# Optimization experiments

Hardware: AMD Instinct MI355X
Metric: run time of the kernel (lower is better)

Reference implementation:

```python
import jax, jax.numpy as jnp
import numpy as np

B, N, C = 4, 8192, 512
H, D = 8, 64          # heads, dim_head; inner_dim = H*D = 512
EPS = 1e-6


def setup_inputs() -> dict:
    key = jax.random.key(0)
    k1, k2, k3 = jax.random.split(key, 3)
    x = jax.random.normal(k1, (B, N, C), dtype=jnp.float32)
    # fan-in scaled init so sigmoid features are not saturated
    W_qkv = jax.random.normal(k2, (3 * H * D, C), dtype=jnp.float32) * (C ** -0.5)
    W_proj = jax.random.normal(k3, (C, H * D), dtype=jnp.float32) * ((H * D) ** -0.5)
    b_proj = jnp.zeros((C,), dtype=jnp.float32)
    return {"x": x, "W_qkv": W_qkv, "W_proj": W_proj, "b_proj": b_proj}


def reference(x, W_qkv, W_proj, b_proj):
    b, n, c = x.shape
    qkv = x @ W_qkv.T                                   # [B,N,3HD]
    q, k, v = jnp.split(qkv, 3, axis=-1)
    to_heads = lambda t: t.reshape(b, n, H, D).transpose(0, 2, 1, 3)  # [B,H,N,D]
    q, k, v = to_heads(q), to_heads(k), to_heads(v)
    q = jax.nn.sigmoid(q)
    k = jax.nn.sigmoid(k)
    scale = D ** -0.5
    v = v / ((scale * c) // H)                           # torch: v / (scale*C // heads) == v / 8.0

    k_sum = k.sum(axis=2)                                # [B,H,D]
    q_sum = q.sum(axis=2)                                # [B,H,D]
    # sink/source incoming-outgoing flow (per token): [B,H,N]
    sink_incoming = 1.0 / (((q + EPS) * (k_sum + EPS)[:, :, None, :]).sum(-1) + EPS)
    source_outgoing = 1.0 / (((k + EPS) * (q_sum + EPS)[:, :, None, :]).sum(-1) + EPS)
    conserved_sink = ((q + EPS) * ((k * source_outgoing[..., None]).sum(2) + EPS)[:, :, None, :]).sum(-1) + EPS
    conserved_source = ((k + EPS) * ((q * sink_incoming[..., None]).sum(2) + EPS)[:, :, None, :]).sum(-1) + EPS
    conserved_source = jnp.clip(conserved_source, -1.0, 1.0)

    sink_allocation = jax.nn.sigmoid(conserved_sink * (float(q.shape[2]) / float(k.shape[2])))
    source_competition = jax.nn.softmax(conserved_source, axis=-1) * float(k.shape[2])

    # linear attention: k^T @ v then q @ (kv); kv is tiny [B,H,D,D]
    kv = jnp.einsum('bhnd,bhne->bhde', k, v * source_competition[..., None])
    x_update = jnp.einsum('bhnd,bhde->bhne', q, kv) * sink_incoming[..., None] * sink_allocation[..., None]

    out = x_update.transpose(0, 2, 1, 3).reshape(b, n, H * D)
    return out @ W_proj.T + b_proj
```

## Files before the change

### kernel.cpp

```cpp
#include <hip/hip_runtime.h>
#include <hip/hip_bf16.h>

typedef __attribute__((ext_vector_type(8))) short short8;
typedef __attribute__((ext_vector_type(4))) float f32x4;

constexpr int cB = 4, cN = 8192, cC = 512, cH = 8, cD = 64;
constexpr int cM = cB * cN;
constexpr int cHD = cH * cD;
constexpr int cBH = cB * cH;
constexpr float kEPS = 1e-6f;
constexpr int KV_SPLIT = 32;

__device__ __forceinline__ ushort rne_bf16(float f) {
  unsigned u = __float_as_uint(f);
  u += 0x7fffu + ((u >> 16) & 1u);
  return (ushort)(u >> 16);
}
__device__ __forceinline__ float b2f(ushort u) {
  return __uint_as_float((unsigned)u << 16);
}

__global__ __launch_bounds__(256) void round_w(const float* __restrict__ src,
    ushort* __restrict__ w, int n4) {
  int i = blockIdx.x * 256 + threadIdx.x;
  if (i >= n4) return;
  float4 v = reinterpret_cast<const float4*>(src)[i];
  ushort4 h;
  h.x = rne_bf16(v.x); h.y = rne_bf16(v.y);
  h.z = rne_bf16(v.z); h.w = rne_bf16(v.w);
  reinterpret_cast<ushort4*>(w)[i] = h;
}

template<int EPI, int NY>
__global__ __launch_bounds__(256) void gemm_mfma(
    const ushort* __restrict__ Ab, const ushort* __restrict__ Wb, int bstride,
    const float* __restrict__ bias,
    void* __restrict__ o0v, void* __restrict__ o1v, void* __restrict__ o2v,
    float* __restrict__ qsum, float* __restrict__ ksum) {
  constexpr int NT = cC / 32;
  __shared__ ushort AhS[2][128 * 32];
  __shared__ ushort BhS[2][128 * 32];
  float* colsum = (float*)AhS;
  const int t = threadIdx.x;
  const int wave = t >> 6, lane = t & 63;
  const int wm = wave >> 1, wn = wave & 1;
  const int l15 = lane & 15, lg = lane >> 4;

  const int raw = blockIdx.y * gridDim.x + blockIdx.x;
  const int q8 = (int)(gridDim.x * NY) >> 3;
  const int wg2 = (raw & 7) * q8 + (raw >> 3);
  const int rowchunk = wg2 / NY, ycol = wg2 - rowchunk * NY;
  const int row0 = rowchunk * 128, col0 = ycol * 128;
  const size_t wofs = (size_t)(row0 >> 13) * (size_t)bstride;

  f32x4 acc[4][4] = {};

  const int srow = lane >> 2, sunit = lane & 3;

#define STAGE_T(basep, base0, dstbuf, k0)                                       \
  _Pragma("unroll")                                                             \
  for (int hh = 0; hh < 2; ++hh) {                                              \
    const int rr_ = wave * 32 + hh * 16 + srow;                                 \
    const int sw = sunit ^ ((rr_ >> 1) & 3);                                    \
    const size_t goff = (size_t)(base0 + rr_) * cC + (k0) + sw * 8;             \
    __builtin_amdgcn_global_load_lds(                                           \
        (const __attribute__((address_space(1))) void*)(basep + goff),          \
        (__attribute__((address_space(3))) void*)(&dstbuf[(wave * 32 + hh * 16) * 32]), \
        16, 0, 0);                                                              \
  }

  STAGE_T(Ab, row0, AhS[0], 0);
  STAGE_T((Wb + wofs), col0, BhS[0], 0);
  STAGE_T(Ab, row0, AhS[1], 32);
  STAGE_T((Wb + wofs), col0, BhS[1], 32);

  int cur = 0;
  for (int kt = 0; kt < NT; ++kt) {
    if (kt < NT - 1) asm volatile("s_waitcnt vmcnt(4)" ::: "memory");
    else             asm volatile("s_waitcnt vmcnt(0)" ::: "memory");
    __builtin_amdgcn_s_barrier();
    short8 ah[4], bhf[4];
    #pragma unroll
    for (int mi = 0; mi < 4; ++mi) {
      const int r = wm * 64 + mi * 16 + l15;
      ah[mi] = *reinterpret_cast<const short8*>(
          &AhS[cur][r * 32 + (lg ^ ((r >> 1) & 3)) * 8]);
    }
    #pragma unroll
    for (int ni = 0; ni < 4; ++ni) {
      const int c = wn * 64 + ni * 16 + l15;
      bhf[ni] = *reinterpret_cast<const short8*>(
          &BhS[cur][c * 32 + (lg ^ ((c >> 1) & 3)) * 8]);
    }
    asm volatile("s_waitcnt lgkmcnt(0)" ::: "memory");
    __builtin_amdgcn_sched_barrier(0);
    __builtin_amdgcn_s_barrier();
    if (kt + 2 < NT) {
      STAGE_T(Ab, row0, AhS[cur], (kt + 2) * 32);
      STAGE_T((Wb + wofs), col0, BhS[cur], (kt + 2) * 32);
    }
    #pragma unroll
    for (int ni = 0; ni < 4; ++ni)
      #pragma unroll
      for (int mi = 0; mi < 4; ++mi)
        acc[mi][ni] = __builtin_amdgcn_mfma_f32_16x16x32_bf16(ah[mi], bhf[ni], acc[mi][ni], 0, 0, 0);
    cur ^= 1;
  }
#undef STAGE_T

  const bool qk_block = (EPI == 0) && (ycol < 8);
  if (qk_block) {
    if (t < 128) colsum[t] = 0.f;
    __syncthreads();
  }

  float csum[4] = {};
  #pragma unroll
  for (int mi = 0; mi < 4; ++mi) {
    #pragma unroll
    for (int r = 0; r < 4; ++r) {
      const int m = row0 + wm * 64 + mi * 16 + lg * 4 + r;
      #pragma unroll
      for (int ni = 0; ni < 4; ++ni) {
        const int col = col0 + wn * 64 + ni * 16 + l15;
        const float val = acc[mi][ni][r];
        if (EPI == 0) {
          const int which = col >> 9;
          const int c2 = col & 511;
          const int h = c2 >> 6, d = c2 & 63;
          const int bb = m >> 13, n = m & 8191;
          const size_t idx = (((size_t)(bb * cH + h)) * cN + n) * cD + d;
          if (which < 2) {
            const float sv = 1.f / (1.f + __expf(-val));
            if (which == 0) ((ushort*)o0v)[idx] = rne_bf16(sv);
            else            ((ushort*)o1v)[idx] = rne_bf16(sv);
            csum[ni] += sv;
          } else {
            ((ushort*)o2v)[idx] = rne_bf16(val * 0.125f);
          }
        } else {
          ((float*)o0v)[(size_t)m * cC + col] = val + bias[col];
        }
      }
    }
  }
  if (qk_block) {
    #pragma unroll
    for (int ni = 0; ni < 4; ++ni)
      atomicAdd(&colsum[wn * 64 + ni * 16 + l15], csum[ni]);
    __syncthreads();
    if (t < 128) {
      const int col = col0 + t;
      const int c2 = col & 511;
      const int h = c2 >> 6, d = c2 & 63;
      const int bb = row0 >> 13;
      float* tgt = (col < 512) ? qsum : ksum;
      atomicAdd(&tgt[(bb * cH + h) * cD + d], colsum[t]);
    }
  }
}

__global__ __launch_bounds__(256) void k34_flow(const ushort* __restrict__ q,
      const ushort* __restrict__ k, const float* __restrict__ qsum,
      const float* __restrict__ ksum, float* __restrict__ si,
      float* __restrict__ Sq, float* __restrict__ Sk) {
  const int bh = blockIdx.x;
  const int n0 = blockIdx.y * 256;
  const int t = threadIdx.x;
  const int wave = t >> 6, lane = t & 63;
  const int g = lane >> 4, j = lane & 15;
  const ushort* qb = q + (size_t)bh * cN * cD;
  const ushort* kb = k + (size_t)bh * cN * cD;
  const float4 ks4 = *(const float4*)&ksum[bh * 64 + j * 4];
  const float4 qs4 = *(const float4*)&qsum[bh * 64 + j * 4];
  const float ksd[4] = {ks4.x + kEPS, ks4.y + kEPS, ks4.z + kEPS, ks4.w + kEPS};
  const float qsd[4] = {qs4.x + kEPS, qs4.y + kEPS, qs4.z + kEPS, qs4.w + kEPS};
  float aSq[4] = {}, aSk[4] = {};
  for (int i = 0; i < 16; ++i) {
    const int n = n0 + wave * 64 + i * 4 + g;
    const ushort4 qu = *(const ushort4*)&qb[(size_t)n * cD + j * 4];
    const ushort4 ku = *(const ushort4*)&kb[(size_t)n * cD + j * 4];
    const float qa[4] = {b2f(qu.x), b2f(qu.y), b2f(qu.z), b2f(qu.w)};
    const float ka[4] = {b2f(ku.x), b2f(ku.y), b2f(ku.z), b2f(ku.w)};
    float t1 = 0.f, t2 = 0.f;
    #pragma unroll
    for (int c = 0; c < 4; ++c) {
      t1 = fmaf(qa[c] + kEPS, ksd[c], t1);
      t2 = fmaf(ka[c] + kEPS, qsd[c], t2);
    }
    #pragma unroll
    for (int off = 1; off < 16; off <<= 1) {
      t1 += __shfl_xor(t1, off);
      t2 += __shfl_xor(t2, off);
    }
    const float si_n = 1.f / (t1 + kEPS);
    const float so_n = 1.f / (t2 + kEPS);
    if (j == 0) si[(size_t)bh * cN + n] = si_n;
    #pragma unroll
    for (int c = 0; c < 4; ++c) {
      aSq[c] = fmaf(qa[c], si_n, aSq[c]);
      aSk[c] = fmaf(ka[c], so_n, aSk[c]);
    }
  }
  #pragma unroll
  for (int c = 0; c < 4; ++c) {
    aSq[c] += __shfl_xor(aSq[c], 16); aSq[c] += __shfl_xor(aSq[c], 32);
    aSk[c] += __shfl_xor(aSk[c], 16); aSk[c] += __shfl_xor(aSk[c], 32);
  }
  __shared__ float sAq[4][64], sAk[4][64];
  if (g == 0) {
    #pragma unroll
    for (int c = 0; c < 4; ++c) { sAq[wave][j * 4 + c] = aSq[c]; sAk[wave][j * 4 + c] = aSk[c]; }
  }
  __syncthreads();
  if (t < 64) {
    atomicAdd(&Sq[bh * 64 + t], sAq[0][t] + sAq[1][t] + sAq[2][t] + sAq[3][t]);
    atomicAdd(&Sk[bh * 64 + t], sAk[0][t] + sAk[1][t] + sAk[2][t] + sAk[3][t]);
  }
}

__global__ __launch_bounds__(256) void k45_kv(const ushort* __restrict__ kk_,
      const ushort* __restrict__ vv, const float* __restrict__ Sq,
      float* __restrict__ kvpart, float* __restrict__ zpart) {
  const int bh = blockIdx.x;
  const int y = blockIdx.y;
  constexpr int ROWS = cN / KV_SPLIT;
  const int n0 = y * ROWS;
  const int t = threadIdx.x;
  const int d = t & 63, eb = t >> 6;
  const int g = t >> 4, j = t & 15;
  const int sr = t >> 4, sc = (t & 15) * 4;
  const ushort* kb = kk_ + (size_t)bh * cN * cD;
  const ushort* vb = vv + (size_t)bh * cN * cD;
  const float4 sq4 = *(const float4*)&Sq[bh * 64 + j * 4];
  const float SqE[4] = {sq4.x + kEPS, sq4.y + kEPS, sq4.z + kEPS, sq4.w + kEPS};
  __shared__ float ks[32][64];
  __shared__ float vs[32][64];
  __shared__ float evs[32];
  __shared__ float zl[16];
  float acc[16] = {};
  float zacc = 0.f;
  ushort4 pk0 = *(const ushort4*)&kb[(size_t)(n0 + sr) * cD + sc];
  ushort4 pk1 = *(const ushort4*)&kb[(size_t)(n0 + 16 + sr) * cD + sc];
  ushort4 pv0 = *(const ushort4*)&vb[(size_t)(n0 + sr) * cD + sc];
  ushort4 pv1 = *(const ushort4*)&vb[(size_t)(n0 + 16 + sr) * cD + sc];
  for (int c0 = 0; c0 < ROWS; c0 += 32) {
    __syncthreads();
    *(float4*)&ks[sr][sc]      = make_float4(b2f(pk0.x), b2f(pk0.y), b2f(pk0.z), b2f(pk0.w));
    *(float4*)&ks[sr + 16][sc] = make_float4(b2f(pk1.x), b2f(pk1.y), b2f(pk1.z), b2f(pk1.w));
    *(float4*)&vs[sr][sc]      = make_float4(b2f(pv0.x), b2f(pv0.y), b2f(pv0.z), b2f(pv0.w));
    *(float4*)&vs[sr + 16][sc] = make_float4(b2f(pv1.x), b2f(pv1.y), b2f(pv1.z), b2f(pv1.w));
    __syncthreads();
    if (c0 + 32 < ROWS) {
      pk0 = *(const ushort4*)&kb[(size_t)(n0 + c0 + 32 + sr) * cD + sc];
      pk1 = *(const ushort4*)&kb[(size_t)(n0 + c0 + 48 + sr) * cD + sc];
      pv0 = *(const ushort4*)&vb[(size_t)(n0 + c0 + 32 + sr) * cD + sc];
      pv1 = *(const ushort4*)&vb[(size_t)(n0 + c0 + 48 + sr) * cD + sc];
    }
    #pragma unroll
    for (int rr = 0; rr < 2; ++rr) {
      const int r = g * 2 + rr;
      const float4 kk4 = *(const float4*)&ks[r][j * 4];
      float tt = 0.f;
      tt = fmaf(kk4.x + kEPS, SqE[0], tt);
      tt = fmaf(kk4.y + kEPS, SqE[1], tt);
      tt = fmaf(kk4.z + kEPS, SqE[2], tt);
      tt = fmaf(kk4.w + kEPS, SqE[3], tt);
      #pragma unroll
      for (int off = 1; off < 16; off <<= 1) tt += __shfl_xor(tt, off);
      if (j == 0) {
        const float cs = fminf(fmaxf(tt + kEPS, -1.f), 1.f);
        const float e = __expf(cs);
        evs[r] = e;
        zacc += e;
      }
    }
    __syncthreads();
    #pragma unroll
    for (int r = 0; r < 32; ++r) {
      const float kd = ks[r][d] * evs[r];
      #pragma unroll
      for (int j2 = 0; j2 < 16; ++j2)
        acc[j2] = fmaf(kd, vs[r][eb * 16 + j2], acc[j2]);
    }
  }
  if (j == 0) zl[g] = zacc;
  __syncthreads();
  if (t == 0) {
    float z = 0.f;
    #pragma unroll
    for (int i = 0; i < 16; ++i) z += zl[i];
    zpart[y * cBH + bh] = z;
  }
  float* kvb = kvpart + ((size_t)y * cBH + bh) * 4096 + d * 64 + eb * 16;
  #pragma unroll
  for (int j2 = 0; j2 < 16; ++j2) kvb[j2] = acc[j2];
}

__global__ __launch_bounds__(256) void k5r_reduce(const float* __restrict__ kvpart,
      const float* __restrict__ zpart, float* __restrict__ kvm, float* __restrict__ Zb) {
  const int bh = blockIdx.x;
  const int yq = blockIdx.y;
  const int t = threadIdx.x;
  for (int i = yq * 1024 + t; i < (yq + 1) * 1024; i += 256) {
    float s = 0.f;
    #pragma unroll
    for (int yy = 0; yy < KV_SPLIT; ++yy)
      s += kvpart[((size_t)yy * cBH + bh) * 4096 + i];
    kvm[(size_t)bh * 4096 + i] = s;
  }
  if (yq == 0 && t == 0) {
    float z = 0.f;
    #pragma unroll
    for (int yy = 0; yy < KV_SPLIT; ++yy) z += zpart[yy * cBH + bh];
    Zb[bh] = z;
  }
}

__global__ __launch_bounds__(256) void kvw_build(const float* __restrict__ kvm,
      const float* __restrict__ Wproj, const float* __restrict__ Zb,
      ushort* __restrict__ kvw) {
  const int bh = blockIdx.x;
  const int c0 = blockIdx.y * 128;
  const int b = bh >> 3, h = bh & 7;
  const int t = threadIdx.x;
  __shared__ float kvs[64][64];
  for (int i = t; i < 4096; i += 256)
    kvs[i >> 6][i & 63] = kvm[(size_t)bh * 4096 + i];
  __syncthreads();
  const float zs = (float)cN / Zb[bh];
  const int cl = t & 127, half = t >> 7;
  const int c = c0 + cl;
  float acc[32] = {};
  for (int ec = 0; ec < 64; ec += 8) {
    float w[8];
    #pragma unroll
    for (int e = 0; e < 8; ++e)
      w[e] = Wproj[(size_t)c * cHD + h * 64 + ec + e];
    #pragma unroll
    for (int d = 0; d < 32; ++d)
      #pragma unroll
      for (int e = 0; e < 8; ++e)
        acc[d] = fmaf(kvs[half * 32 + d][ec + e], w[e], acc[d]);
  }
  ushort* dst = kvw + (size_t)b * cC * cHD + (size_t)c * cC + h * 64 + half * 32;
  #pragma unroll
  for (int d = 0; d < 32; ++d) dst[d] = rne_bf16(acc[d] * zs);
}

__global__ __launch_bounds__(256) void k6c_scaleq(const ushort* __restrict__ q,
      const float* __restrict__ si, const float* __restrict__ Sk,
      ushort* __restrict__ xq) {
  const int bh = blockIdx.x;
  const int b = bh >> 3, head = bh & 7;
  const int n0 = blockIdx.y * 256;
  const int t = threadIdx.x;
  const int wave = t >> 6, lane = t & 63;
  const int g = lane >> 4, j = lane & 15;
  const ushort* qb = q + (size_t)bh * cN * cD;
  const float4 sk4 = *(const float4*)&Sk[bh * 64 + j * 4];
  const float SkE[4] = {sk4.x + kEPS, sk4.y + kEPS, sk4.z + kEPS, sk4.w + kEPS};
  for (int i = 0; i < 16; ++i) {
    const int n = n0 + wave * 64 + i * 4 + g;
    const ushort4 qu = *(const ushort4*)&qb[(size_t)n * cD + j * 4];
    const float q0 = b2f(qu.x), q1 = b2f(qu.y), q2 = b2f(qu.z), q3 = b2f(qu.w);
    float t2 = 0.f;
    t2 = fmaf(q0 + kEPS, SkE[0], t2);
    t2 = fmaf(q1 + kEPS, SkE[1], t2);
    t2 = fmaf(q2 + kEPS, SkE[2], t2);
    t2 = fmaf(q3 + kEPS, SkE[3], t2);
    #pragma unroll
    for (int off = 1; off < 16; off <<= 1) t2 += __shfl_xor(t2, off);
    const float sa_n = 1.f / (1.f + __expf(-(t2 + kEPS)));
    const float s = si[(size_t)bh * cN + n] * sa_n;
    ushort4 hh;
    hh.x = rne_bf16(q0 * s);
    hh.y = rne_bf16(q1 * s);
    hh.z = rne_bf16(q2 * s);
    hh.w = rne_bf16(q3 * s);
    const size_t m = (size_t)b * cN + n;
    *(ushort4*)&xq[m * cC + head * 64 + j * 4] = hh;
  }
}

extern "C" void kernel_launch(void* const* d_in, const int* in_sizes, int n_in,
                              void* d_out, int out_size, void* d_ws, size_t ws_size,
                              hipStream_t stream) {
  (void)in_sizes; (void)n_in; (void)out_size;
  const float* x     = (const float*)d_in[0];
  const float* Wqkv  = (const float*)d_in[1];
  const float* Wproj = (const float*)d_in[2];
  const float* bproj = (const float*)d_in[3];
  float* out = (float*)d_out;
  float* ws  = (float*)d_ws;

  const size_t SLAB = (size_t)cBH * cN * cD;
  const size_t OFF_Q   = 0;
  const size_t OFF_K   = SLAB;
  const size_t OFF_V   = 2 * SLAB;
  const size_t OFF_ACC = 3 * SLAB;
  const size_t ACC_FLOATS = 2048 * 4 + 32 + (size_t)cBH * cD * cD;
  const size_t OFF_R   = OFF_ACC + ACC_FLOATS;
  const size_t R_FLOATS = (size_t)3 * cHD * cC;
  const size_t TOTAL   = OFF_R + R_FLOATS;
  if (ws_size < TOTAL * sizeof(float)) return;

  ushort* q16 = (ushort*)(ws + OFF_Q);
  ushort* k16 = (ushort*)(ws + OFF_K);
  ushort* v16 = (ushort*)(ws + OFF_V);
  ushort* xq  = (ushort*)(ws + OFF_V + SLAB / 2);
  float* ksum = ws + OFF_ACC;
  float* qsum = ksum + 2048;
  float* Sk   = ksum + 4096;
  float* Sq   = ksum + 6144;
  float* Zb   = ksum + 8192;
  float* kvm  = ksum + 8224;

  ushort* wq  = (ushort*)(ws + OFF_R);
  float*  si  = ws + OFF_R;
  ushort* kvw = (ushort*)(ws + OFF_R + (size_t)cBH * cN);

  ushort* xs    = (ushort*)out;
  float* kvpart = out + (size_t)8 * 1024 * 1024;
  float* zpart  = kvpart + (size_t)KV_SPLIT * cBH * 4096;

  hipMemsetAsync(ksum, 0, ACC_FLOATS * sizeof(float), stream);

  round_w<<<(3 * cHD * cC / 4 + 255) / 256, 256, 0, stream>>>(Wqkv, wq, 3 * cHD * cC / 4);
  round_w<<<((size_t)cM * cC / 4 + 255) / 256, 256, 0, stream>>>(x, xs, cM * cC / 4);
  gemm_mfma<0, 12><<<dim3(cM / 128, (3 * cHD) / 128), 256, 0, stream>>>(
      xs, wq, 0, nullptr, q16, k16, v16, qsum, ksum);
  k34_flow<<<dim3(cBH, cN / 256), 256, 0, stream>>>(q16, k16, qsum, ksum, si, Sq, Sk);
  k45_kv<<<dim3(cBH, KV_SPLIT), 256, 0, stream>>>(k16, v16, Sq, kvpart, zpart);
  k5r_reduce<<<dim3(cBH, 4), 256, 0, stream>>>(kvpart, zpart, kvm, Zb);
  kvw_build<<<dim3(cBH, 4), 256, 0, stream>>>(kvm, Wproj, Zb, kvw);
  k6c_scaleq<<<dim3(cBH, cN / 256), 256, 0, stream>>>(q16, si, Sk, xq);
  gemm_mfma<1, 4><<<dim3(cM / 128, cHD / 128), 256, 0, stream>>>(
      xq, kvw, cC * cHD, bproj, out, nullptr, nullptr, nullptr, nullptr);
}
```

Before: 238.2 us.

## Give each wave private LDS tiles to remove block barriers in GEMM loop

Each wave now stages its own 64-row A slice and 64-column B slice into a private LDS region, replacing the shared double-buffered 128x32 tiles and the two block-wide barriers per K step. Because waves share no data, only a vmcnt wait is needed before reading, and the next tile is prefetched after the LDS reads finish. The cost is that A and B tiles are fetched twice each (paired waves duplicate loads), global traffic per block doubles, and only one stage of prefetch remains, so load latency is less hidden.

```diff
diff --git a/kernel.cpp b/kernel.cpp
--- a/kernel.cpp
+++ b/kernel.cpp
@@ -38,9 +38,8 @@
     void* __restrict__ o0v, void* __restrict__ o1v, void* __restrict__ o2v,
     float* __restrict__ qsum, float* __restrict__ ksum) {
   constexpr int NT = cC / 32;
-  __shared__ ushort AhS[2][128 * 32];
-  __shared__ ushort BhS[2][128 * 32];
-  float* colsum = (float*)AhS;
+  __shared__ ushort LDSu[4 * 4096];
+  float* colsum = (float*)LDSu;
   const int t = threadIdx.x;
   const int wave = t >> 6, lane = t & 63;
   const int wm = wave >> 1, wn = wave & 1;
@@ -56,60 +55,60 @@
   f32x4 acc[4][4] = {};
 
   const int srow = lane >> 2, sunit = lane & 3;
-
-#define STAGE_T(basep, base0, dstbuf, k0)                                       \
+  const int agbase = row0 + wm * 64;
+  const int bgbase = col0 + wn * 64;
+  const ushort* Wp = Wb + wofs;
+  ushort* Apriv = &LDSu[wave * 4096];
+  ushort* Bpriv = &LDSu[wave * 4096 + 2048];
+
+#define STAGE_PRIV(basep, gbase, dstp, k0)                                      \
   _Pragma("unroll")                                                             \
-  for (int hh = 0; hh < 2; ++hh) {                                              \
-    const int rr_ = wave * 32 + hh * 16 + srow;                                 \
-    const int sw = sunit ^ ((rr_ >> 1) & 3);                                    \
-    const size_t goff = (size_t)(base0 + rr_) * cC + (k0) + sw * 8;             \
+  for (int cc = 0; cc < 4; ++cc) {                                              \
+    const int lr = cc * 16 + srow;                                              \
+    const int sw = sunit ^ ((lr >> 1) & 3);                                     \
+    const size_t goff = (size_t)(gbase + lr) * cC + (k0) + sw * 8;              \
     __builtin_amdgcn_global_load_lds(                                           \
         (const __attribute__((address_space(1))) void*)(basep + goff),          \
-        (__attribute__((address_space(3))) void*)(&dstbuf[(wave * 32 + hh * 16) * 32]), \
+        (__attribute__((address_space(3))) void*)(&dstp[cc * 512]),             \
         16, 0, 0);                                                              \
   }
 
-  STAGE_T(Ab, row0, AhS[0], 0);
-  STAGE_T((Wb + wofs), col0, BhS[0], 0);
-  STAGE_T(Ab, row0, AhS[1], 32);
-  STAGE_T((Wb + wofs), col0, BhS[1], 32);
-
-  int cur = 0;
+  STAGE_PRIV(Ab, agbase, Apriv, 0);
+  STAGE_PRIV(Wp, bgbase, Bpriv, 0);
+
   for (int kt = 0; kt < NT; ++kt) {
-    if (kt < NT - 1) asm volatile("s_waitcnt vmcnt(4)" ::: "memory");
-    else             asm volatile("s_waitcnt vmcnt(0)" ::: "memory");
-    __builtin_amdgcn_s_barrier();
+    asm volatile("s_waitcnt vmcnt(0)" ::: "memory");
+    __builtin_amdgcn_sched_barrier(0);
     short8 ah[4], bhf[4];
     #pragma unroll
     for (int mi = 0; mi < 4; ++mi) {
-      const int r = wm * 64 + mi * 16 + l15;
+      const int r = mi * 16 + l15;
       ah[mi] = *reinterpret_cast<const short8*>(
-          &AhS[cur][r * 32 + (lg ^ ((r >> 1) & 3)) * 8]);
+          &Apriv[r * 32 + (lg ^ ((r >> 1) & 3)) * 8]);
     }
     #pragma unroll
     for (int ni = 0; ni < 4; ++ni) {
-      const int c = wn * 64 + ni * 16 + l15;
+      const int c = ni * 16 + l15;
       bhf[ni] = *reinterpret_cast<const short8*>(
-          &BhS[cur][c * 32 + (lg ^ ((c >> 1) & 3)) * 8]);
+          &Bpriv[c * 32 + (lg ^ ((c >> 1) & 3)) * 8]);
     }
     asm volatile("s_waitcnt lgkmcnt(0)" ::: "memory");
     __builtin_amdgcn_sched_barrier(0);
-    __builtin_amdgcn_s_barrier();
-    if (kt + 2 < NT) {
-      STAGE_T(Ab, row0, AhS[cur], (kt + 2) * 32);
-      STAGE_T((Wb + wofs), col0, BhS[cur], (kt + 2) * 32);
+    if (kt + 1 < NT) {
+      STAGE_PRIV(Ab, agbase, Apriv, (kt + 1) * 32);
+      STAGE_PRIV(Wp, bgbase, Bpriv, (kt + 1) * 32);
     }
     #pragma unroll
     for (int ni = 0; ni < 4; ++ni)
       #pragma unroll
       for (int mi = 0; mi < 4; ++mi)
         acc[mi][ni] = __builtin_amdgcn_mfma_f32_16x16x32_bf16(ah[mi], bhf[ni], acc[mi][ni], 0, 0, 0);
-    cur ^= 1;
-  }
-#undef STAGE_T
+  }
+#undef STAGE_PRIV
 
   const bool qk_block = (EPI == 0) && (ycol < 8);
   if (qk_block) {
+    __syncthreads();
     if (t < 128) colsum[t] = 0.f;
     __syncthreads();
   }
```

After: 265.1 us. 11.3% more time.
